# Kernel optimization log

Hardware: AMD Instinct MI355X
Metric: run time of the kernel (lower is better)

Reference implementation:

```python
import jax, jax.numpy as jnp
import numpy as np

B, T, E, H, S = 4, 4096, 1024, 16, 64
D = E // H  # head_dim = 64
ROPE_BASE = 10000.0


def _rotate_half(x):
    # interleaved rotate: out[..., 2i] = -x[..., 2i+1]; out[..., 2i+1] = x[..., 2i]
    x1 = x[..., ::2]
    x2 = x[..., 1::2]
    return jnp.stack([-x2, x1], axis=-1).reshape(x.shape)


def _rope_cos_sin(t, d):
    inv_freq = 1.0 / (ROPE_BASE ** (jnp.arange(0, d, 2, dtype=jnp.float32) / d))
    freqs = jnp.arange(t, dtype=jnp.float32)[:, None] * inv_freq[None, :]  # [t, d/2]
    emb = jnp.concatenate([freqs, freqs], axis=-1)  # [t, d]
    # broadcast over batch and heads for q/k of shape [b, t, h, d]
    return jnp.cos(emb)[None, :, None, :], jnp.sin(emb)[None, :, None, :]


def setup_inputs() -> dict:
    key = jax.random.key(0)
    ks = jax.random.split(key, 6)
    s = E ** -0.5
    return {
        "x": jax.random.normal(ks[0], (B, T, E), dtype=jnp.float32),
        "Wq": jax.random.normal(ks[1], (E, E), dtype=jnp.float32) * s,
        "Wk": jax.random.normal(ks[2], (E, E), dtype=jnp.float32) * s,
        "Wv": jax.random.normal(ks[3], (E, E), dtype=jnp.float32) * s,
        "Wout": jax.random.normal(ks[4], (E, E), dtype=jnp.float32) * s,
        "slot_keys": jax.random.normal(ks[5], (H, S, D), dtype=jnp.float32) * (D ** -0.5),
    }


def reference(x, Wq, Wk, Wv, Wout, slot_keys):
    b, t, e = x.shape
    h, s_slots, d = slot_keys.shape
    scale = d ** -0.5

    q = (x @ Wq.T).reshape(b, t, h, d)
    k = (x @ Wk.T).reshape(b, t, h, d)
    v = (x @ Wv.T).reshape(b, t, h, d)

    cos, sin = _rope_cos_sin(t, d)
    q = q * cos + _rotate_half(q) * sin
    k = k * cos + _rotate_half(k) * sin

    # write pass: route each token's value into memory slots
    write_logits = jnp.einsum('bthd,hsd->bths', k, slot_keys) * scale
    write_weights = jax.nn.softmax(write_logits, axis=-1)  # write_temperature = 1.0
    slot_state = jnp.einsum('bths,bthd->bshd', write_weights, v) / t

    # read pass: query the slot memory
    read_logits = jnp.einsum('bthd,bshd->bths', q, slot_state) * scale
    read_weights = jax.nn.softmax(read_logits, axis=-1)  # read_temperature = 1.0
    read_out = jnp.einsum('bths,bshd->bthd', read_weights, slot_state)

    return read_out.reshape(b, t, e) @ Wout.T
```

## Files before the change

kernel.cpp:

```cpp
#include <hip/hip_runtime.h>
#include <cstdint>
#include <cstddef>

#define BB 4
#define TT 4096
#define EE 1024
#define HH 16
#define SSLOTS 64
#define DD 64
#define MM (BB*TT)

typedef unsigned short u16;
typedef __attribute__((ext_vector_type(8))) short s16x8;
typedef __attribute__((ext_vector_type(4))) float f32x4;
typedef __attribute__((ext_vector_type(8))) unsigned short us8v;
typedef __attribute__((ext_vector_type(4))) unsigned short us4v;

#define MFMA16(a, b, c) __builtin_amdgcn_mfma_f32_16x16x32_bf16((a), (b), (c), 0, 0, 0)

__device__ __forceinline__ u16 f2bf(float x) {
  union { float f; uint32_t u; } c; c.f = x;
  uint32_t u = c.u;
  u += 0x7fffu + ((u >> 16) & 1u);
  return (u16)(u >> 16);
}

__device__ __forceinline__ float bf2f(u16 x) {
  union { uint32_t u; float f; } c; c.u = ((uint32_t)x) << 16;
  return c.f;
}

__device__ __forceinline__ void async16(const void* g, void* l) {
  auto lp = reinterpret_cast<__attribute__((address_space(3))) void*>(
      reinterpret_cast<uintptr_t>(l));
  auto gp = reinterpret_cast<const __attribute__((address_space(1))) void*>(
      reinterpret_cast<uintptr_t>(g));
  __builtin_amdgcn_global_load_lds(gp, lp, 16, 0, 0);
}

__device__ __forceinline__ us8v rope8(us8v kv, const float* __restrict__ rcp,
                                      const float* __restrict__ rsp) {
  float e[8];
#pragma unroll
  for (int m = 0; m < 8; ++m) e[m] = bf2f((u16)kv[m]);
  us8v o;
#pragma unroll
  for (int j = 0; j < 4; ++j) {
    float c0 = rcp[2 * j], c1 = rcp[2 * j + 1];
    float s0 = rsp[2 * j], s1 = rsp[2 * j + 1];
    o[2 * j]     = f2bf(e[2 * j] * c0 - e[2 * j + 1] * s0);
    o[2 * j + 1] = f2bf(e[2 * j + 1] * c1 + e[2 * j] * s1);
  }
  return o;
}

__global__ __launch_bounds__(256) void k_prep(const float* __restrict__ x,
                                              const float* __restrict__ w0,
                                              const float* __restrict__ w1,
                                              const float* __restrict__ w2,
                                              const float* __restrict__ w3,
                                              u16* __restrict__ x16,
                                              u16* __restrict__ dW,
                                              u16* __restrict__ dWo,
                                              float* __restrict__ rc,
                                              float* __restrict__ rs) {
  int bid = blockIdx.x;
  if (bid < 16384) {
    int i = (bid * 256 + threadIdx.x) * 4;
    float4 v = *(const float4*)(x + i);
    us4v o = { f2bf(v.x), f2bf(v.y), f2bf(v.z), f2bf(v.w) };
    *(us4v*)(x16 + i) = o;
  } else if (bid < 16384 + 4096) {
    int bb = bid - 16384;
    int sel = bb >> 10;
    const float* s = (sel == 0) ? w0 : (sel == 1) ? w1 : (sel == 2) ? w2 : w3;
    u16* d = (sel < 3) ? (dW + (size_t)sel * EE * EE) : dWo;
    int i = ((bb & 1023) * 256 + threadIdx.x) * 4;
    float4 v = *(const float4*)(s + i);
    us4v o = { f2bf(v.x), f2bf(v.y), f2bf(v.z), f2bf(v.w) };
    *(us4v*)(d + i) = o;
  } else {
    int i = (bid - 16384 - 4096) * 256 + threadIdx.x;
    int t = i >> 5, f = i & 31;
    double invf = pow(10000.0, -(double)(2 * f) / 64.0);
    double th = fmod((double)t * invf, 6.28318530717958647692528676655900577);
    rc[i] = (float)cos(th);
    rs[i] = (float)sin(th);
  }
}


__device__ __forceinline__ void mm16(f32x4 (&acc)[8][4], const s16x8* a,
                                     const s16x8* b, int ab) {
#pragma unroll
  for (int im = 0; im < 4; ++im)
#pragma unroll
    for (int in = 0; in < 4; ++in)
      acc[ab + im][in] = MFMA16(a[im], b[in], acc[ab + im][in]);
}

__device__ __forceinline__ void gemm256(const u16* __restrict__ A,
                                        const u16* __restrict__ B,
                                        char* smem, f32x4 (&acc)[8][4]) {
  const int tid = threadIdx.x, lane = tid & 63, wave = tid >> 6;
  const int l16 = lane & 15, q4 = lane >> 4;
  const int wrow = (wave >> 2) * 128;
  const int wcol = (wave & 3) * 64;

  const int sr0 = wave * 32 + (lane >> 2);
  const int sr1 = sr0 + 16;
  const int sc  = (lane & 3) * 16;
  const size_t ga0 = (size_t)sr0 * 2048 + (size_t)(sc ^ (((sr0 >> 1) & 3) << 4));
  const size_t ga1 = (size_t)sr1 * 2048 + (size_t)(sc ^ (((sr1 >> 1) & 3) << 4));
  const int lo0 = sr0 * 64 + sc;
  const int lo1 = sr1 * 64 + sc;
  const char* Ab = (const char*)A;
  const char* Bb = (const char*)B;

  int offA[8], offB[4];
#pragma unroll
  for (int f = 0; f < 8; ++f) {
    int r = wrow + f * 16 + l16;
    offA[f] = (r * 64 + q4 * 16) ^ (((r >> 1) & 3) << 4);
  }
#pragma unroll
  for (int f = 0; f < 4; ++f) {
    int r = wcol + f * 16 + l16;
    offB[f] = (r * 64 + q4 * 16) ^ (((r >> 1) & 3) << 4);
  }

#define STG(dst, srcb, kb) do { \
    async16((srcb) + (size_t)(kb) + ga0, (dst) + lo0); \
    async16((srcb) + (size_t)(kb) + ga1, (dst) + lo1); } while (0)

  STG(smem +     0, Ab, 0);
  STG(smem + 32768, Bb, 0);
  STG(smem + 16384, Ab, 64);
  STG(smem + 49152, Bb, 64);
  STG(smem + 65536 +     0, Ab, 128);
  STG(smem + 65536 + 32768, Bb, 128);
  asm volatile("s_waitcnt vmcnt(4)" ::: "memory");
  __builtin_amdgcn_s_barrier();

  for (int tau = 0; tau < 16; ++tau) {
    char* cb = smem + ((tau & 1) << 16);
    char* nb = smem + (((tau + 1) & 1) << 16);
    const char* Ak0 = cb;
    const char* Ak1 = cb + 16384;
    const char* Bk0 = cb + 32768;
    const char* Bk1 = cb + 49152;
    const int kb1 = (tau + 1) << 7;
    const int kb2 = (tau + 2) << 7;
    const bool st1 = tau < 15, st2 = tau < 14;

    s16x8 a[4], b[4];

#pragma unroll
    for (int f = 0; f < 4; ++f) a[f] = *(const s16x8*)(Ak0 + offA[f]);
#pragma unroll
    for (int f = 0; f < 4; ++f) b[f] = *(const s16x8*)(Bk0 + offB[f]);
    if (st1) STG(nb + 16384, Ab, kb1 + 64);
    __builtin_amdgcn_s_barrier();
    asm volatile("s_waitcnt lgkmcnt(0)" ::: "memory");
    __builtin_amdgcn_s_setprio(1);
    mm16(acc, a, b, 0);
    __builtin_amdgcn_s_setprio(0);
    __builtin_amdgcn_s_barrier();

#pragma unroll
    for (int f = 0; f < 4; ++f) a[f] = *(const s16x8*)(Ak0 + offA[4 + f]);
    if (st1) STG(nb + 49152, Bb, kb1 + 64);
    if (st2) asm volatile("s_waitcnt vmcnt(6)" ::: "memory");
    else     asm volatile("s_waitcnt vmcnt(0)" ::: "memory");
    __builtin_amdgcn_s_barrier();
    asm volatile("s_waitcnt lgkmcnt(0)" ::: "memory");
    __builtin_amdgcn_s_setprio(1);
    mm16(acc, a, b, 4);
    __builtin_amdgcn_s_setprio(0);
    __builtin_amdgcn_s_barrier();

#pragma unroll
    for (int f = 0; f < 4; ++f) a[f] = *(const s16x8*)(Ak1 + offA[f]);
#pragma unroll
    for (int f = 0; f < 4; ++f) b[f] = *(const s16x8*)(Bk1 + offB[f]);
    if (st2) STG(cb, Ab, kb2);
    __builtin_amdgcn_s_barrier();
    asm volatile("s_waitcnt lgkmcnt(0)" ::: "memory");
    __builtin_amdgcn_s_setprio(1);
    mm16(acc, a, b, 0);
    __builtin_amdgcn_s_setprio(0);
    __builtin_amdgcn_s_barrier();

#pragma unroll
    for (int f = 0; f < 4; ++f) a[f] = *(const s16x8*)(Ak1 + offA[4 + f]);
    if (st2) STG(cb + 32768, Bb, kb2);
    if (st2) asm volatile("s_waitcnt vmcnt(6)" ::: "memory");
    else     asm volatile("s_waitcnt vmcnt(0)" ::: "memory");
    __builtin_amdgcn_s_barrier();
    asm volatile("s_waitcnt lgkmcnt(0)" ::: "memory");
    __builtin_amdgcn_s_setprio(1);
    mm16(acc, a, b, 4);
    __builtin_amdgcn_s_setprio(0);
    __builtin_amdgcn_s_barrier();
  }
#undef STG
}

__global__ __launch_bounds__(512, 2) void k_gemm_qkv(const u16* __restrict__ A,
                                                     const u16* __restrict__ Bw,
                                                     u16* __restrict__ q16,
                                                     u16* __restrict__ k16,
                                                     u16* __restrict__ v16) {
  __shared__ char smem[131072];
  const int bid = blockIdx.x;
  const int xcd = bid & 7, local = bid >> 3;
  const int mt = xcd * 8 + (local & 7);
  const int nt = local >> 3;
  const int m0 = mt * 256, n0 = nt * 256;

  f32x4 acc[8][4];
#pragma unroll
  for (int i = 0; i < 8; ++i)
#pragma unroll
    for (int j = 0; j < 4; ++j) acc[i][j] = (f32x4){0.f, 0.f, 0.f, 0.f};

  gemm256(A + (size_t)m0 * 1024, Bw + (size_t)n0 * 1024, smem, acc);

  const int tid = threadIdx.x, lane = tid & 63, wave = tid >> 6;
  const int l16 = lane & 15, q4 = lane >> 4;
  const int wrow = (wave >> 2) * 128, wn = (wave & 3) * 64;
  const int which = n0 >> 10;
  const int nbl = n0 & 1023;
  u16* dst = (which == 0) ? q16 : ((which == 1) ? k16 : v16);

#pragma unroll
  for (int im = 0; im < 8; ++im)
#pragma unroll
    for (int in = 0; in < 4; ++in)
#pragma unroll
      for (int reg = 0; reg < 4; ++reg) {
        float v = acc[im][in][reg];
        int m = m0 + wrow + im * 16 + q4 * 4 + reg;
        int nn = nbl + wn + in * 16 + l16;
        int bq = m >> 12, t = m & 4095;
        int h = nn >> 6, d = nn & 63;
        dst[((size_t)(bq * HH + h) * TT + t) * 64 + d] = f2bf(v);
      }
}

__global__ __launch_bounds__(512, 2) void k_gemm_out(const u16* __restrict__ A,
                                                     const u16* __restrict__ Bw,
                                                     float* __restrict__ C) {
  __shared__ char smem[131072];
  const int bid = blockIdx.x;
  const int xcd = bid & 7, local = bid >> 3;
  const int mt = xcd * 8 + (local & 7);
  const int nt = local >> 3;
  const int m0 = mt * 256, n0 = nt * 256;

  f32x4 acc[8][4];
#pragma unroll
  for (int i = 0; i < 8; ++i)
#pragma unroll
    for (int j = 0; j < 4; ++j) acc[i][j] = (f32x4){0.f, 0.f, 0.f, 0.f};

  gemm256(A + (size_t)m0 * 1024, Bw + (size_t)n0 * 1024, smem, acc);

  const int tid = threadIdx.x, lane = tid & 63, wave = tid >> 6;
  const int l16 = lane & 15, q4 = lane >> 4;
  const int wrow = (wave >> 2) * 128, wn = (wave & 3) * 64;
#pragma unroll
  for (int im = 0; im < 8; ++im)
#pragma unroll
    for (int in = 0; in < 4; ++in)
#pragma unroll
      for (int reg = 0; reg < 4; ++reg) {
        int m = m0 + wrow + im * 16 + q4 * 4 + reg;
        int n = n0 + wn + in * 16 + l16;
        C[(size_t)m * 1024 + n] = acc[im][in][reg];
      }
}

__global__ __launch_bounds__(256) void k_stage2(const u16* __restrict__ K16g,
                                                const u16* __restrict__ V16g,
                                                const float* __restrict__ SKg,
                                                const float* __restrict__ rc,
                                                const float* __restrict__ rs,
                                                float* __restrict__ SSb) {
  const int tid = threadIdx.x, lane = tid & 63, wave = tid >> 6;
  const int l16 = lane & 15, q4 = lane >> 4, q8 = q4 * 8;
  const int bh = blockIdx.x >> 3, cb = blockIdx.x & 7;
  const int h = bh & 15;

  __shared__ u16 Ks[128 * 88];
  __shared__ u16 Vs[64 * 136];
  __shared__ u16 SKs[64 * 88];
  u16* ww = Ks;

  const float* skh = SKg + (size_t)h * (SSLOTS * DD);
  for (int i = tid; i < 4096; i += 256)
    SKs[(i >> 6) * 88 + (i & 63)] = f2bf(skh[i]);

  f32x4 a2[4];
#pragma unroll
  for (int in = 0; in < 4; ++in) a2[in] = (f32x4){0.f, 0.f, 0.f, 0.f};

  const int w32 = wave * 32;
  for (int cc = 0; cc < 4; ++cc) {
    const int tg0 = cb * 512 + cc * 128;
    __syncthreads();

    const u16* ks = K16g + ((size_t)bh * TT + tg0) * 64;
    for (int idx = tid; idx < 1024; idx += 256) {
      int t = idx >> 3, p = idx & 7;
      us8v kv = *(const us8v*)(ks + (size_t)t * 64 + p * 8);
      int fi = (tg0 + t) * 32 + ((p * 8) & 31);
      us8v kr = rope8(kv, rc + fi, rs + fi);
      *(us8v*)&Ks[t * 88 + p * 8] = kr;
    }
    const u16* vsrc = V16g + ((size_t)bh * TT + tg0) * 64;
    for (int idx = tid; idx < 1024; idx += 256) {
      int t = idx & 127, dg = idx >> 7;
      us8v vv = *(const us8v*)(vsrc + (size_t)t * 64 + dg * 8);
#pragma unroll
      for (int j = 0; j < 8; ++j) Vs[(dg * 8 + j) * 136 + t] = vv[j];
    }
    __syncthreads();

    f32x4 a1[2][4];
#pragma unroll
    for (int im = 0; im < 2; ++im)
#pragma unroll
      for (int in = 0; in < 4; ++in) a1[im][in] = (f32x4){0.f, 0.f, 0.f, 0.f};
#pragma unroll
    for (int ksx = 0; ksx < 2; ++ksx) {
      s16x8 afr0 = *(const s16x8*)&Ks[(w32 + l16) * 88 + ksx * 32 + q8];
      s16x8 afr1 = *(const s16x8*)&Ks[(w32 + 16 + l16) * 88 + ksx * 32 + q8];
#pragma unroll
      for (int in = 0; in < 4; ++in) {
        s16x8 bfr = *(const s16x8*)&SKs[(in * 16 + l16) * 88 + ksx * 32 + q8];
        a1[0][in] = MFMA16(afr0, bfr, a1[0][in]);
        a1[1][in] = MFMA16(afr1, bfr, a1[1][in]);
      }
    }
    __syncthreads();

#pragma unroll
    for (int im = 0; im < 2; ++im)
#pragma unroll
      for (int reg = 0; reg < 4; ++reg) {
        float v0 = a1[im][0][reg] * 0.125f, v1 = a1[im][1][reg] * 0.125f;
        float v2 = a1[im][2][reg] * 0.125f, v3 = a1[im][3][reg] * 0.125f;
        float mx = fmaxf(fmaxf(v0, v1), fmaxf(v2, v3));
#pragma unroll
        for (int m = 1; m < 16; m <<= 1) mx = fmaxf(mx, __shfl_xor(mx, m));
        float e0 = __expf(v0 - mx), e1 = __expf(v1 - mx);
        float e2 = __expf(v2 - mx), e3 = __expf(v3 - mx);
        float sm = e0 + e1 + e2 + e3;
#pragma unroll
        for (int m = 1; m < 16; m <<= 1) sm += __shfl_xor(sm, m);
        float inv = 1.0f / sm;
        int tl = w32 + im * 16 + q4 * 4 + reg;
        ww[(l16) * 136 + tl]      = f2bf(e0 * inv);
        ww[(16 + l16) * 136 + tl] = f2bf(e1 * inv);
        ww[(32 + l16) * 136 + tl] = f2bf(e2 * inv);
        ww[(48 + l16) * 136 + tl] = f2bf(e3 * inv);
      }
    __syncthreads();

#pragma unroll
    for (int ksx = 0; ksx < 4; ++ksx) {
      s16x8 afr = *(const s16x8*)&ww[(wave * 16 + l16) * 136 + ksx * 32 + q8];
#pragma unroll
      for (int in = 0; in < 4; ++in) {
        s16x8 bfr = *(const s16x8*)&Vs[(in * 16 + l16) * 136 + ksx * 32 + q8];
        a2[in] = MFMA16(afr, bfr, a2[in]);
      }
    }
  }

  const float invT = 1.0f / (float)TT;
#pragma unroll
  for (int in = 0; in < 4; ++in)
#pragma unroll
    for (int reg = 0; reg < 4; ++reg) {
      int s = wave * 16 + q4 * 4 + reg;
      int d = in * 16 + l16;
      atomicAdd(&SSb[(size_t)bh * 4096 + s * 64 + d], a2[in][reg] * invT);
    }
}

__global__ __launch_bounds__(256) void k_stage3(const u16* __restrict__ Q16g,
                                                const float* __restrict__ SSg,
                                                const float* __restrict__ rc,
                                                const float* __restrict__ rs,
                                                u16* __restrict__ RO) {
  const int tid = threadIdx.x, lane = tid & 63, wave = tid >> 6;
  const int l16 = lane & 15, q4 = lane >> 4, q8 = q4 * 8;
  const int bh = blockIdx.x >> 5, ck = blockIdx.x & 31;
  const int b = bh >> 4, h = bh & 15;
  const int tg0 = ck * 128;

  __shared__ u16 Qs[128 * 88];
  __shared__ u16 ss_sd[64 * 88];
  __shared__ u16 ss_ds[64 * 88];
  u16* RWs = Qs;

  const float* ssp = SSg + (size_t)bh * 4096;
  for (int i = tid; i < 4096; i += 256) {
    u16 u = f2bf(ssp[i]);
    int s = i >> 6, d = i & 63;
    ss_sd[s * 88 + d] = u;
    ss_ds[d * 88 + s] = u;
  }
  const u16* qsrc = Q16g + ((size_t)bh * TT + tg0) * 64;
  for (int idx = tid; idx < 1024; idx += 256) {
    int t = idx >> 3, p = idx & 7;
    us8v qv = *(const us8v*)(qsrc + (size_t)t * 64 + p * 8);
    int fi = (tg0 + t) * 32 + ((p * 8) & 31);
    us8v qr = rope8(qv, rc + fi, rs + fi);
    *(us8v*)&Qs[t * 88 + p * 8] = qr;
  }
  __syncthreads();

  const int w32 = wave * 32;
  f32x4 a3[2][4];
#pragma unroll
  for (int i = 0; i < 2; ++i)
#pragma unroll
    for (int j = 0; j < 4; ++j) a3[i][j] = (f32x4){0.f, 0.f, 0.f, 0.f};
#pragma unroll
  for (int ksx = 0; ksx < 2; ++ksx) {
    s16x8 afr[2];
#pragma unroll
    for (int im = 0; im < 2; ++im)
      afr[im] = *(const s16x8*)&Qs[(w32 + im * 16 + l16) * 88 + ksx * 32 + q8];
#pragma unroll
    for (int in = 0; in < 4; ++in) {
      s16x8 bfr = *(const s16x8*)&ss_sd[(in * 16 + l16) * 88 + ksx * 32 + q8];
#pragma unroll
      for (int im = 0; im < 2; ++im) a3[im][in] = MFMA16(afr[im], bfr, a3[im][in]);
    }
  }
  __syncthreads();

#pragma unroll
  for (int im = 0; im < 2; ++im)
#pragma unroll
    for (int reg = 0; reg < 4; ++reg) {
      float v0 = a3[im][0][reg] * 0.125f, v1 = a3[im][1][reg] * 0.125f;
      float v2 = a3[im][2][reg] * 0.125f, v3 = a3[im][3][reg] * 0.125f;
      float mx = fmaxf(fmaxf(v0, v1), fmaxf(v2, v3));
#pragma unroll
      for (int m = 1; m < 16; m <<= 1) mx = fmaxf(mx, __shfl_xor(mx, m));
      float e0 = __expf(v0 - mx), e1 = __expf(v1 - mx);
      float e2 = __expf(v2 - mx), e3 = __expf(v3 - mx);
      float sm = e0 + e1 + e2 + e3;
#pragma unroll
      for (int m = 1; m < 16; m <<= 1) sm += __shfl_xor(sm, m);
      float inv = 1.0f / sm;
      int tl = w32 + im * 16 + q4 * 4 + reg;
      RWs[tl * 88 + l16]      = f2bf(e0 * inv);
      RWs[tl * 88 + 16 + l16] = f2bf(e1 * inv);
      RWs[tl * 88 + 32 + l16] = f2bf(e2 * inv);
      RWs[tl * 88 + 48 + l16] = f2bf(e3 * inv);
    }
  __syncthreads();

  f32x4 a4[2][4];
#pragma unroll
  for (int i = 0; i < 2; ++i)
#pragma unroll
    for (int j = 0; j < 4; ++j) a4[i][j] = (f32x4){0.f, 0.f, 0.f, 0.f};
#pragma unroll
  for (int ksx = 0; ksx < 2; ++ksx) {
    s16x8 afr[2];
#pragma unroll
    for (int im = 0; im < 2; ++im)
      afr[im] = *(const s16x8*)&RWs[(w32 + im * 16 + l16) * 88 + ksx * 32 + q8];
#pragma unroll
    for (int in = 0; in < 4; ++in) {
      s16x8 bfr = *(const s16x8*)&ss_ds[(in * 16 + l16) * 88 + ksx * 32 + q8];
#pragma unroll
      for (int im = 0; im < 2; ++im) a4[im][in] = MFMA16(afr[im], bfr, a4[im][in]);
    }
  }

#pragma unroll
  for (int im = 0; im < 2; ++im)
#pragma unroll
    for (int in = 0; in < 4; ++in)
#pragma unroll
      for (int reg = 0; reg < 4; ++reg) {
        int t = tg0 + w32 + im * 16 + q4 * 4 + reg;
        int d = in * 16 + l16;
        RO[((size_t)b * TT + t) * 1024 + h * 64 + d] = f2bf(a4[im][in][reg]);
      }
}

extern "C" void kernel_launch(void* const* d_in, const int* in_sizes, int n_in,
                              void* d_out, int out_size, void* d_ws, size_t ws_size,
                              hipStream_t stream) {
  const float* x  = (const float*)d_in[0];
  const float* Wq = (const float*)d_in[1];
  const float* Wk = (const float*)d_in[2];
  const float* Wv = (const float*)d_in[3];
  const float* Wo = (const float*)d_in[4];
  const float* SK = (const float*)d_in[5];
  float* out = (float*)d_out;

  char* w = (char*)d_ws;
  u16* x16 = (u16*)w;   w += (size_t)MM * EE * 2;
  u16* W16 = (u16*)w;   w += (size_t)3 * EE * EE * 2;
  u16* Wo16 = (u16*)w;  w += (size_t)EE * EE * 2;
  u16* Q16 = (u16*)w;   w += (size_t)BB * HH * TT * DD * 2;
  u16* K16 = (u16*)w;   w += (size_t)BB * HH * TT * DD * 2;
  u16* V16 = (u16*)w;   w += (size_t)BB * HH * TT * DD * 2;
  float* SSb = (float*)w; w += (size_t)BB * HH * SSLOTS * DD * 4;
  float* rc = (float*)w;  w += (size_t)TT * 32 * 4;
  float* rs = (float*)w;  w += (size_t)TT * 32 * 4;
  u16* RO16 = x16;

  if ((size_t)(w - (char*)d_ws) > ws_size) return;

  k_prep<<<16384 + 4096 + 512, 256, 0, stream>>>(x, Wq, Wk, Wv, Wo, x16, W16, Wo16, rc, rs);

  k_gemm_qkv<<<768, 512, 0, stream>>>(x16, W16, Q16, K16, V16);

  hipMemsetAsync(SSb, 0, (size_t)BB * HH * SSLOTS * DD * 4, stream);
  k_stage2<<<512, 256, 0, stream>>>(K16, V16, SK, rc, rs, SSb);
  k_stage3<<<2048, 256, 0, stream>>>(Q16, SSb, rc, rs, RO16);

  k_gemm_out<<<256, 512, 0, stream>>>(RO16, Wo16, out);
}
```

Measured before the change: 333.1 us.

## Fuse RoPE into QKV GEMM epilogue and emit transposed V via LDS staging

The QKV GEMM epilogue now applies RoPE to Q and K in fp32 before bf16 rounding, using a lane shuffle to get the pair partner. It stages the output tile in swizzled shared memory so global stores are 16-byte vectors instead of scattered 2-byte writes. V is written pre-transposed ([bh][d][t]), so stage2 loads it with vector copies instead of a scalar LDS transpose, and stage2/stage3 drop their RoPE work. The cost is extra rc/rs loads and an LDS round trip with a barrier in the GEMM epilogue. RoPE is now applied before bf16 rounding, which changes numerics slightly.

```diff
diff --git a/kernel.cpp b/kernel.cpp
--- a/kernel.cpp
+++ b/kernel.cpp
@@ -36,22 +36,6 @@
   auto gp = reinterpret_cast<const __attribute__((address_space(1))) void*>(
       reinterpret_cast<uintptr_t>(g));
   __builtin_amdgcn_global_load_lds(gp, lp, 16, 0, 0);
-}
-
-__device__ __forceinline__ us8v rope8(us8v kv, const float* __restrict__ rcp,
-                                      const float* __restrict__ rsp) {
-  float e[8];
-#pragma unroll
-  for (int m = 0; m < 8; ++m) e[m] = bf2f((u16)kv[m]);
-  us8v o;
-#pragma unroll
-  for (int j = 0; j < 4; ++j) {
-    float c0 = rcp[2 * j], c1 = rcp[2 * j + 1];
-    float s0 = rsp[2 * j], s1 = rsp[2 * j + 1];
-    o[2 * j]     = f2bf(e[2 * j] * c0 - e[2 * j + 1] * s0);
-    o[2 * j + 1] = f2bf(e[2 * j + 1] * c1 + e[2 * j] * s1);
-  }
-  return o;
 }
 
 __global__ __launch_bounds__(256) void k_prep(const float* __restrict__ x,
@@ -208,9 +192,11 @@
 
 __global__ __launch_bounds__(512, 2) void k_gemm_qkv(const u16* __restrict__ A,
                                                      const u16* __restrict__ Bw,
+                                                     const float* __restrict__ rc,
+                                                     const float* __restrict__ rs,
                                                      u16* __restrict__ q16,
                                                      u16* __restrict__ k16,
-                                                     u16* __restrict__ v16) {
+                                                     u16* __restrict__ v16t) {
   __shared__ char smem[131072];
   const int bid = blockIdx.x;
   const int xcd = bid & 7, local = bid >> 3;
@@ -231,21 +217,60 @@
   const int wrow = (wave >> 2) * 128, wn = (wave & 3) * 64;
   const int which = n0 >> 10;
   const int nbl = n0 & 1023;
-  u16* dst = (which == 0) ? q16 : ((which == 1) ? k16 : v16);
-
-#pragma unroll
-  for (int im = 0; im < 8; ++im)
-#pragma unroll
-    for (int in = 0; in < 4; ++in)
-#pragma unroll
-      for (int reg = 0; reg < 4; ++reg) {
-        float v = acc[im][in][reg];
-        int m = m0 + wrow + im * 16 + q4 * 4 + reg;
-        int nn = nbl + wn + in * 16 + l16;
-        int bq = m >> 12, t = m & 4095;
-        int h = nn >> 6, d = nn & 63;
-        dst[((size_t)(bq * HH + h) * TT + t) * 64 + d] = f2bf(v);
+  const int bq = m0 >> 12, t0 = m0 & 4095;
+  u16* sm = (u16*)smem;
+
+  if (which < 2) {
+    u16* dst = (which == 0) ? q16 : k16;
+#pragma unroll
+    for (int im = 0; im < 8; ++im)
+#pragma unroll
+      for (int in = 0; in < 4; ++in)
+#pragma unroll
+        for (int reg = 0; reg < 4; ++reg) {
+          float v = acc[im][in][reg];
+          float p = __shfl_xor(v, 1);
+          int tl = wrow + im * 16 + q4 * 4 + reg;
+          int d = in * 16 + l16;
+          int fi = (t0 + tl) * 32 + (d >> 1);
+          float c = rc[fi], s = rs[fi];
+          float r = (d & 1) ? (v * c + p * s) : (v * c - p * s);
+          int nn = wn + in * 16 + l16;
+          sm[tl * 256 + (nn ^ ((tl & 7) << 3))] = f2bf(r);
+        }
+    __syncthreads();
+#pragma unroll
+    for (int it = 0; it < 16; ++it) {
+      int idx = (it * 512 + tid) * 8;
+      int tl = idx >> 8, n = idx & 255;
+      us8v val = *(const us8v*)&sm[tl * 256 + (n ^ ((tl & 7) << 3))];
+      int h = (nbl + n) >> 6, d = n & 63;
+      *(us8v*)&dst[((size_t)(bq * HH + h) * TT + t0 + tl) * 64 + d] = val;
+    }
+  } else {
+#pragma unroll
+    for (int im = 0; im < 8; ++im)
+#pragma unroll
+      for (int in = 0; in < 4; ++in) {
+        int tl0 = wrow + im * 16 + q4 * 4;
+        int n = wn + in * 16 + l16;
+        us4v pk = { f2bf(acc[im][in][0]), f2bf(acc[im][in][1]),
+                    f2bf(acc[im][in][2]), f2bf(acc[im][in][3]) };
+        *(us4v*)&sm[n * 256 + (tl0 ^ ((n & 7) << 2))] = pk;
       }
+    __syncthreads();
+#pragma unroll
+    for (int it = 0; it < 16; ++it) {
+      int idx = (it * 512 + tid) * 8;
+      int n = idx >> 8, tl = idx & 255;
+      int x = (n & 7) << 2;
+      us4v lo = *(const us4v*)&sm[n * 256 + ((tl + 0) ^ x)];
+      us4v hi = *(const us4v*)&sm[n * 256 + ((tl + 4) ^ x)];
+      us8v val = { lo[0], lo[1], lo[2], lo[3], hi[0], hi[1], hi[2], hi[3] };
+      int h = (nbl + n) >> 6, d = n & 63;
+      *(us8v*)&v16t[((size_t)(bq * HH + h) * DD + d) * TT + t0 + tl] = val;
+    }
+  }
 }
 
 __global__ __launch_bounds__(512, 2) void k_gemm_out(const u16* __restrict__ A,
@@ -282,10 +307,8 @@
 }
 
 __global__ __launch_bounds__(256) void k_stage2(const u16* __restrict__ K16g,
-                                                const u16* __restrict__ V16g,
+                                                const u16* __restrict__ V16t,
                                                 const float* __restrict__ SKg,
-                                                const float* __restrict__ rc,
-                                                const float* __restrict__ rs,
                                                 float* __restrict__ SSb) {
   const int tid = threadIdx.x, lane = tid & 63, wave = tid >> 6;
   const int l16 = lane & 15, q4 = lane >> 4, q8 = q4 * 8;
@@ -313,17 +336,12 @@
     const u16* ks = K16g + ((size_t)bh * TT + tg0) * 64;
     for (int idx = tid; idx < 1024; idx += 256) {
       int t = idx >> 3, p = idx & 7;
-      us8v kv = *(const us8v*)(ks + (size_t)t * 64 + p * 8);
-      int fi = (tg0 + t) * 32 + ((p * 8) & 31);
-      us8v kr = rope8(kv, rc + fi, rs + fi);
-      *(us8v*)&Ks[t * 88 + p * 8] = kr;
-    }
-    const u16* vsrc = V16g + ((size_t)bh * TT + tg0) * 64;
+      *(us8v*)&Ks[t * 88 + p * 8] = *(const us8v*)(ks + (size_t)t * 64 + p * 8);
+    }
+    const u16* vsrc = V16t + (size_t)bh * DD * TT + tg0;
     for (int idx = tid; idx < 1024; idx += 256) {
-      int t = idx & 127, dg = idx >> 7;
-      us8v vv = *(const us8v*)(vsrc + (size_t)t * 64 + dg * 8);
-#pragma unroll
-      for (int j = 0; j < 8; ++j) Vs[(dg * 8 + j) * 136 + t] = vv[j];
+      int d = idx >> 4, c8 = (idx & 15) * 8;
+      *(us8v*)&Vs[d * 136 + c8] = *(const us8v*)(vsrc + (size_t)d * TT + c8);
     }
     __syncthreads();
 
@@ -392,8 +410,6 @@
 
 __global__ __launch_bounds__(256) void k_stage3(const u16* __restrict__ Q16g,
                                                 const float* __restrict__ SSg,
-                                                const float* __restrict__ rc,
-                                                const float* __restrict__ rs,
                                                 u16* __restrict__ RO) {
   const int tid = threadIdx.x, lane = tid & 63, wave = tid >> 6;
   const int l16 = lane & 15, q4 = lane >> 4, q8 = q4 * 8;
@@ -416,10 +432,7 @@
   const u16* qsrc = Q16g + ((size_t)bh * TT + tg0) * 64;
   for (int idx = tid; idx < 1024; idx += 256) {
     int t = idx >> 3, p = idx & 7;
-    us8v qv = *(const us8v*)(qsrc + (size_t)t * 64 + p * 8);
-    int fi = (tg0 + t) * 32 + ((p * 8) & 31);
-    us8v qr = rope8(qv, rc + fi, rs + fi);
-    *(us8v*)&Qs[t * 88 + p * 8] = qr;
+    *(us8v*)&Qs[t * 88 + p * 8] = *(const us8v*)(qsrc + (size_t)t * 64 + p * 8);
   }
   __syncthreads();
 
@@ -515,7 +528,7 @@
   u16* Wo16 = (u16*)w;  w += (size_t)EE * EE * 2;
   u16* Q16 = (u16*)w;   w += (size_t)BB * HH * TT * DD * 2;
   u16* K16 = (u16*)w;   w += (size_t)BB * HH * TT * DD * 2;
-  u16* V16 = (u16*)w;   w += (size_t)BB * HH * TT * DD * 2;
+  u16* V16t = (u16*)w;  w += (size_t)BB * HH * TT * DD * 2;
   float* SSb = (float*)w; w += (size_t)BB * HH * SSLOTS * DD * 4;
   float* rc = (float*)w;  w += (size_t)TT * 32 * 4;
   float* rs = (float*)w;  w += (size_t)TT * 32 * 4;
@@ -525,11 +538,11 @@
 
   k_prep<<<16384 + 4096 + 512, 256, 0, stream>>>(x, Wq, Wk, Wv, Wo, x16, W16, Wo16, rc, rs);
 
-  k_gemm_qkv<<<768, 512, 0, stream>>>(x16, W16, Q16, K16, V16);
+  k_gemm_qkv<<<768, 512, 0, stream>>>(x16, W16, rc, rs, Q16, K16, V16t);
 
   hipMemsetAsync(SSb, 0, (size_t)BB * HH * SSLOTS * DD * 4, stream);
-  k_stage2<<<512, 256, 0, stream>>>(K16, V16, SK, rc, rs, SSb);
-  k_stage3<<<2048, 256, 0, stream>>>(Q16, SSb, rc, rs, RO16);
+  k_stage2<<<512, 256, 0, stream>>>(K16, V16t, SK, SSb);
+  k_stage3<<<2048, 256, 0, stream>>>(Q16, SSb, RO16);
 
   k_gemm_out<<<256, 512, 0, stream>>>(RO16, Wo16, out);
 }
```

Measured after the change: 349.4 us. +4.9%, slower.
